# Kernel tuning notes

Measured on AMD Instinct MI355X. Metric: run time of the kernel, lower is better.

## Reference

```python
import jax, jax.numpy as jnp
import numpy as np

KERNEL_MUL = 2.0
KERNEL_NUM = 5


def setup_inputs() -> dict:
    key = jax.random.key(0)
    k1, k2 = jax.random.split(key)
    N, D = 4096, 512
    source = jax.random.normal(k1, (N, D), dtype=jnp.float32)
    target = jax.random.normal(k2, (N, D), dtype=jnp.float32)
    return {"source": source, "target": target}


def _mmd(source, target):
    n = source.shape[0]
    total = jnp.concatenate([source, target], axis=0)  # [2N, D]
    # pairwise squared L2 via the ||a||^2 + ||b||^2 - 2 a.b identity (same math,
    # avoids materializing the [2N,2N,D] expanded tensor the torch code builds)
    sq = jnp.sum(total * total, axis=1)  # [2N]
    L2 = sq[:, None] + sq[None, :] - 2.0 * (total @ total.T)  # [2N, 2N]
    m = total.shape[0]
    # torch uses L2_distance.data -> detached bandwidth
    bandwidth = jax.lax.stop_gradient(jnp.sum(L2)) / (m * m - m)
    bandwidth = bandwidth / (KERNEL_MUL ** (KERNEL_NUM // 2))
    kernels = jnp.zeros_like(L2)
    for i in range(KERNEL_NUM):
        kernels = kernels + jnp.exp(-L2 / (bandwidth * (KERNEL_MUL ** i)))
    XX = kernels[:n, :n]
    YY = kernels[n:, n:]
    XY = kernels[:n, n:]
    YX = kernels[n:, :n]
    return jnp.mean(XX + YY - XY - YX)


def reference(source, target):
    return _mmd(source, target)
```

## Files before the change

kernel.cpp:

```cpp
#include <hip/hip_runtime.h>
#include <hip/hip_fp8.h>

#define NHALF 4096
#define NROWS 8192
#define D 512
#define BM 128
#define BKB 128
#define NKT (D / BKB)
#define NB (NROWS / BM)
#define NTRI (NB * (NB + 1) / 2)
#define CONV_BLOCKS 256

typedef float f32x4 __attribute__((ext_vector_type(4)));

__device__ __forceinline__ const float* row_ptr(const float* __restrict__ src,
                                                const float* __restrict__ tgt, int r) {
    return (r < NHALF) ? (src + (size_t)r * D) : (tgt + (size_t)(r - NHALF) * D);
}

__global__ __launch_bounds__(256)
void conv_stats(const float* __restrict__ src, const float* __restrict__ tgt,
                unsigned char* __restrict__ tot8, float* __restrict__ sq,
                float* __restrict__ colsum, double* __restrict__ sumsq,
                unsigned* __restrict__ ticket, float* __restrict__ inv16bw_out) {
    __shared__ float cs_lds[4][512];
    __shared__ float wssq[4];
    __shared__ int lastFlag;
    __shared__ double red[256];
    int t = threadIdx.x, l = t & 63, w = t >> 6;
    int rbase = blockIdx.x * 32 + w * 8;

    float cs[8] = {0.f, 0.f, 0.f, 0.f, 0.f, 0.f, 0.f, 0.f};
    float ssq = 0.f;

    for (int rr = 0; rr < 8; ++rr) {
        int r = rbase + rr;
        const float* p = row_ptr(src, tgt, r) + l * 8;
        float4 v0 = *(const float4*)p;
        float4 v1 = *(const float4*)(p + 4);
        union { unsigned long long u; int i2[2]; } q;
        q.i2[0] = __builtin_amdgcn_cvt_pk_fp8_f32(v0.x, v0.y, 0, false);
        q.i2[0] = __builtin_amdgcn_cvt_pk_fp8_f32(v0.z, v0.w, q.i2[0], true);
        q.i2[1] = __builtin_amdgcn_cvt_pk_fp8_f32(v1.x, v1.y, 0, false);
        q.i2[1] = __builtin_amdgcn_cvt_pk_fp8_f32(v1.z, v1.w, q.i2[1], true);
        unsigned dstu = (unsigned)((l & 48) | ((l & 15) ^ (r & 15)));
        *(unsigned long long*)&tot8[(size_t)r * D + dstu * 8] = q.u;

        float s8 = v0.x*v0.x + v0.y*v0.y + v0.z*v0.z + v0.w*v0.w
                 + v1.x*v1.x + v1.y*v1.y + v1.z*v1.z + v1.w*v1.w;
        ssq += s8;
        cs[0] += v0.x; cs[1] += v0.y; cs[2] += v0.z; cs[3] += v0.w;
        cs[4] += v1.x; cs[5] += v1.y; cs[6] += v1.z; cs[7] += v1.w;
        float rsum = s8;
        for (int off = 32; off > 0; off >>= 1) rsum += __shfl_down(rsum, off);
        if (l == 0) sq[r] = rsum;
    }
#pragma unroll
    for (int j = 0; j < 8; ++j) cs_lds[w][l * 8 + j] = cs[j];
    for (int off = 32; off > 0; off >>= 1) ssq += __shfl_down(ssq, off);
    if (l == 0) wssq[w] = ssq;
    __syncthreads();
    int c0 = t * 2;
    float a = cs_lds[0][c0] + cs_lds[1][c0] + cs_lds[2][c0] + cs_lds[3][c0];
    float b = cs_lds[0][c0+1] + cs_lds[1][c0+1] + cs_lds[2][c0+1] + cs_lds[3][c0+1];
    atomicAdd(&colsum[c0], a);
    atomicAdd(&colsum[c0 + 1], b);
    if (t == 0) atomicAdd(sumsq, (double)(wssq[0] + wssq[1] + wssq[2] + wssq[3]));
    __syncthreads();

    if (t == 0) {
        __threadfence();
        unsigned old = atomicAdd(ticket, 1u);
        lastFlag = (old == CONV_BLOCKS - 1) ? 1 : 0;
    }
    __syncthreads();
    if (lastFlag) {
        float ca = atomicAdd(&colsum[t], 0.f);
        float cb = atomicAdd(&colsum[t + 256], 0.f);
        red[t] = (double)ca * ca + (double)cb * cb;
        __syncthreads();
        for (int s = 128; s > 0; s >>= 1) {
            if (t < s) red[t] += red[t + s];
            __syncthreads();
        }
        if (t == 0) {
            double ssqd = atomicAdd(sumsq, 0.0);
            double m = (double)NROWS;
            double sumL2 = 2.0 * m * ssqd - 2.0 * red[0];
            double bw = sumL2 / (m * m - m) / 4.0;
            inv16bw_out[0] = (float)(1.0 / (16.0 * bw));
        }
    }
}

__global__ __launch_bounds__(512, 4)
void mmd_main(const unsigned char* __restrict__ tot8,
              const float* __restrict__ sq, const float* __restrict__ inv16bw_p,
              double* __restrict__ S) {
    int b = blockIdx.x;
    int ti = (b & 7) * (NTRI / 8) + (b >> 3);
    int bi = (int)(64.5f - sqrtf(64.5f * 64.5f - 2.0f * (float)ti));
    if (bi < 0) bi = 0;
    while (bi > 0 && bi * NB - bi * (bi - 1) / 2 > ti) --bi;
    while ((bi + 1) * NB - (bi + 1) * bi / 2 <= ti) ++bi;
    int bj = bi + (ti - (bi * NB - bi * (bi - 1) / 2));

    __shared__ __align__(16) unsigned char As[BM * BKB];
    __shared__ __align__(16) unsigned char Bs[BM * BKB];

    int t = threadIdx.x, l = t & 63, w = t >> 6;
    int wr = w >> 2, wc = w & 3;
    int m = l & 15, kg = l >> 4;

    const unsigned char* ab = tot8 + (size_t)(bi * BM) * D;
    const unsigned char* bb = tot8 + (size_t)(bj * BM) * D;

    f32x4 acc[4][2];
#pragma unroll
    for (int i = 0; i < 4; ++i)
#pragma unroll
        for (int j = 0; j < 2; ++j)
            acc[i][j] = (f32x4){0.f, 0.f, 0.f, 0.f};

    for (int kt = 0; kt < NKT; ++kt) {
        __syncthreads();
#pragma unroll
        for (int i = 0; i < 2; ++i) {
            int g = i * 512 + t;
            int row = g >> 3, ch = g & 7;
            __builtin_amdgcn_global_load_lds(
                (const __attribute__((address_space(1))) void*)(ab + (size_t)row * D + kt * BKB + ch * 16),
                (__attribute__((address_space(3))) void*)(As + g * 16),
                16, 0, 0);
            __builtin_amdgcn_global_load_lds(
                (const __attribute__((address_space(1))) void*)(bb + (size_t)row * D + kt * BKB + ch * 16),
                (__attribute__((address_space(3))) void*)(Bs + g * 16),
                16, 0, 0);
        }
        __syncthreads();

#pragma unroll
        for (int ks = 0; ks < 4; ++ks) {
            long af[4], bfr[2];
#pragma unroll
            for (int fi = 0; fi < 4; ++fi) {
                int row = wr * 64 + fi * 16 + m;
                int unit = (ks * 4 + kg) ^ m;
                af[fi] = *(const long*)&As[row * BKB + unit * 8];
            }
#pragma unroll
            for (int fj = 0; fj < 2; ++fj) {
                int row = wc * 32 + fj * 16 + m;
                int unit = (ks * 4 + kg) ^ m;
                bfr[fj] = *(const long*)&Bs[row * BKB + unit * 8];
            }
#pragma unroll
            for (int fi = 0; fi < 4; ++fi)
#pragma unroll
                for (int fj = 0; fj < 2; ++fj)
                    acc[fi][fj] = __builtin_amdgcn_mfma_f32_16x16x32_fp8_fp8(af[fi], bfr[fj], acc[fi][fj], 0, 0, 0);
        }
    }

    float inv16bw = inv16bw_p[0];
    float coef = ((bi == bj) ? 1.f : 2.f) * (((bi < NB / 2) == (bj < NB / 2)) ? 1.f : -1.f);

    float sqj[2];
#pragma unroll
    for (int fj = 0; fj < 2; ++fj) sqj[fj] = sq[bj * BM + wc * 32 + fj * 16 + m];
    int ib = bi * BM + wr * 64 + kg * 4;

    float local = 0.f;
#pragma unroll
    for (int fi = 0; fi < 4; ++fi) {
        float sqi[4];
#pragma unroll
        for (int j = 0; j < 4; ++j) sqi[j] = sq[ib + fi * 16 + j];
#pragma unroll
        for (int fj = 0; fj < 2; ++fj) {
#pragma unroll
            for (int j = 0; j < 4; ++j) {
                float L2 = sqi[j] + sqj[fj] - 2.f * acc[fi][fj][j];
                float u = __expf(-L2 * inv16bw);
                float ks = u;
                u *= u; ks += u;
                u *= u; ks += u;
                u *= u; ks += u;
                u *= u; ks += u;
                if (bi == bj) {
                    int ig = wr * 64 + fi * 16 + kg * 4 + j;
                    int jg = wc * 32 + fj * 16 + m;
                    if (ig == jg) ks = 5.0f;
                }
                local += ks;
            }
        }
    }
    local *= coef;

    for (int off = 32; off > 0; off >>= 1) local += __shfl_down(local, off);
    __shared__ float wsum[8];
    if (l == 0) wsum[w] = local;
    __syncthreads();
    if (t == 0) {
        float bsum = wsum[0] + wsum[1] + wsum[2] + wsum[3]
                   + wsum[4] + wsum[5] + wsum[6] + wsum[7];
        atomicAdd(S, (double)bsum);
    }
}

__global__ void finalize_kernel(const double* __restrict__ S, float* __restrict__ out) {
    out[0] = (float)(S[0] / ((double)NHALF * (double)NHALF));
}

extern "C" void kernel_launch(void* const* d_in, const int* in_sizes, int n_in,
                              void* d_out, int out_size, void* d_ws, size_t ws_size,
                              hipStream_t stream) {
    const float* src = (const float*)d_in[0];
    const float* tgt = (const float*)d_in[1];
    float* out = (float*)d_out;
    char* ws = (char*)d_ws;

    unsigned char* tot8 = (unsigned char*)ws;
    float*    sq      = (float*)(ws + 4194304);
    float*    colsum  = (float*)(ws + 4194304 + 32768);
    double*   sumsq   = (double*)(ws + 4194304 + 34816);
    double*   S       = (double*)(ws + 4194304 + 34824);
    unsigned* ticket  = (unsigned*)(ws + 4194304 + 34832);
    float*    inv16bw = (float*)(ws + 4194304 + 34836);

    hipMemsetAsync(ws + 4194304 + 32768, 0, 2068, stream);

    conv_stats<<<CONV_BLOCKS, 256, 0, stream>>>(src, tgt, tot8, sq, colsum, sumsq, ticket, inv16bw);
    mmd_main<<<NTRI, 512, 0, stream>>>(tot8, sq, inv16bw, S);
    finalize_kernel<<<1, 1, 0, stream>>>(S, out);
}
```

Before: 74.18 us.

## Keep A row-panel resident in LDS and sweep four B tiles per block

Each block now loads its full 128x512 fp8 A row panel into LDS once and iterates over up to four column tiles of the upper triangle, streaming only B k-slices. The next tile's B staging is overlapped with the previous tile's exp epilogue, and per-block reductions become per-wave atomics. This cuts redundant A global loads and block count (2080 to 544). In exchange it uses 80KB of LDS per block, which lowers occupancy, and adds padding tiles clamped to bj=63 with zero coefficient, so some work is wasted.

```diff
diff --git a/kernel.cpp b/kernel.cpp
--- a/kernel.cpp
+++ b/kernel.cpp
@@ -8,7 +8,8 @@
 #define BKB 128
 #define NKT (D / BKB)
 #define NB (NROWS / BM)
-#define NTRI (NB * (NB + 1) / 2)
+#define TPB 4
+#define NBLK 544
 #define CONV_BLOCKS 256
 
 typedef float f32x4 __attribute__((ext_vector_type(4)));
@@ -98,115 +99,144 @@
               const float* __restrict__ sq, const float* __restrict__ inv16bw_p,
               double* __restrict__ S) {
     int b = blockIdx.x;
-    int ti = (b & 7) * (NTRI / 8) + (b >> 3);
-    int bi = (int)(64.5f - sqrtf(64.5f * 64.5f - 2.0f * (float)ti));
-    if (bi < 0) bi = 0;
-    while (bi > 0 && bi * NB - bi * (bi - 1) / 2 > ti) --bi;
-    while ((bi + 1) * NB - (bi + 1) * bi / 2 <= ti) ++bi;
-    int bj = bi + (ti - (bi * NB - bi * (bi - 1) / 2));
-
-    __shared__ __align__(16) unsigned char As[BM * BKB];
-    __shared__ __align__(16) unsigned char Bs[BM * BKB];
+    int nb = (b & 7) * (NBLK / 8) + (b >> 3);
+    int bi = 0, rem = nb;
+    while (rem >= ((67 - bi) >> 2)) { rem -= (67 - bi) >> 2; ++bi; }
+    int bj0 = bi + rem * 4;
+
+    __shared__ __align__(16) unsigned char Al[BM * D];
+    __shared__ __align__(16) unsigned char Bl[BM * BKB];
 
     int t = threadIdx.x, l = t & 63, w = t >> 6;
     int wr = w >> 2, wc = w & 3;
     int m = l & 15, kg = l >> 4;
 
-    const unsigned char* ab = tot8 + (size_t)(bi * BM) * D;
-    const unsigned char* bb = tot8 + (size_t)(bj * BM) * D;
-
-    f32x4 acc[4][2];
-#pragma unroll
-    for (int i = 0; i < 4; ++i)
-#pragma unroll
-        for (int j = 0; j < 2; ++j)
-            acc[i][j] = (f32x4){0.f, 0.f, 0.f, 0.f};
-
-    for (int kt = 0; kt < NKT; ++kt) {
-        __syncthreads();
+    const unsigned char* ap = tot8 + (size_t)bi * BM * D;
+
+    auto stage_B = [&](const unsigned char* bb, int kt) {
 #pragma unroll
         for (int i = 0; i < 2; ++i) {
             int g = i * 512 + t;
             int row = g >> 3, ch = g & 7;
             __builtin_amdgcn_global_load_lds(
-                (const __attribute__((address_space(1))) void*)(ab + (size_t)row * D + kt * BKB + ch * 16),
-                (__attribute__((address_space(3))) void*)(As + g * 16),
+                (const __attribute__((address_space(1))) void*)(bb + (size_t)row * D + kt * BKB + ch * 16),
+                (__attribute__((address_space(3))) void*)(Bl + g * 16),
                 16, 0, 0);
-            __builtin_amdgcn_global_load_lds(
-                (const __attribute__((address_space(1))) void*)(bb + (size_t)row * D + kt * BKB + ch * 16),
-                (__attribute__((address_space(3))) void*)(Bs + g * 16),
-                16, 0, 0);
-        }
-        __syncthreads();
-
-#pragma unroll
-        for (int ks = 0; ks < 4; ++ks) {
-            long af[4], bfr[2];
-#pragma unroll
-            for (int fi = 0; fi < 4; ++fi) {
-                int row = wr * 64 + fi * 16 + m;
+        }
+    };
+
+    f32x4 acc[4][2];
+#pragma unroll
+    for (int i = 0; i < 4; ++i)
+#pragma unroll
+        for (int j = 0; j < 2; ++j)
+            acc[i][j] = (f32x4){0.f, 0.f, 0.f, 0.f};
+
+#pragma unroll
+    for (int i = 0; i < 8; ++i) {
+        int g = i * 512 + t;
+        int row = g >> 5, ch = g & 31;
+        __builtin_amdgcn_global_load_lds(
+            (const __attribute__((address_space(1))) void*)(ap + (size_t)row * D + ch * 16),
+            (__attribute__((address_space(3))) void*)(Al + g * 16),
+            16, 0, 0);
+    }
+    const unsigned char* bb = tot8 + (size_t)bj0 * BM * D;
+    stage_B(bb, 0);
+    __syncthreads();
+
+    float inv16bw = inv16bw_p[0];
+    float wacc = 0.f;
+
+    auto epilogue = [&](int tile) {
+        int bjv = bj0 + tile;
+        float coef = 0.f;
+        int bjc = bjv;
+        if (bjv <= 63) {
+            coef = ((bi == bjv) ? 1.f : 2.f) * (((bi < 32) == (bjv < 32)) ? 1.f : -1.f);
+        } else bjc = 63;
+        float sqj[2];
+#pragma unroll
+        for (int fj = 0; fj < 2; ++fj) sqj[fj] = sq[bjc * BM + wc * 32 + fj * 16 + m];
+        int ib = bi * BM + wr * 64 + kg * 4;
+        float local = 0.f;
+#pragma unroll
+        for (int fi = 0; fi < 4; ++fi) {
+            float sqi[4];
+#pragma unroll
+            for (int j = 0; j < 4; ++j) sqi[j] = sq[ib + fi * 16 + j];
+#pragma unroll
+            for (int fj = 0; fj < 2; ++fj) {
+#pragma unroll
+                for (int j = 0; j < 4; ++j) {
+                    float L2 = sqi[j] + sqj[fj] - 2.f * acc[fi][fj][j];
+                    float u = __expf(-L2 * inv16bw);
+                    float ks = u;
+                    u *= u; ks += u;
+                    u *= u; ks += u;
+                    u *= u; ks += u;
+                    u *= u; ks += u;
+                    if (bi == bjc) {
+                        int ig = wr * 64 + fi * 16 + kg * 4 + j;
+                        int jg = wc * 32 + fj * 16 + m;
+                        if (ig == jg) ks = 5.0f;
+                    }
+                    local += ks;
+                }
+            }
+        }
+        local *= coef;
+        for (int off = 32; off > 0; off >>= 1) local += __shfl_down(local, off);
+        wacc += local;
+#pragma unroll
+        for (int i = 0; i < 4; ++i)
+#pragma unroll
+            for (int j = 0; j < 2; ++j)
+                acc[i][j] = (f32x4){0.f, 0.f, 0.f, 0.f};
+    };
+
+    for (int tp = 0; tp < TPB; ++tp) {
+        for (int kt = 0; kt < NKT; ++kt) {
+#pragma unroll
+            for (int ks = 0; ks < 4; ++ks) {
+                long af[4], bfr[2];
                 int unit = (ks * 4 + kg) ^ m;
-                af[fi] = *(const long*)&As[row * BKB + unit * 8];
+#pragma unroll
+                for (int fi = 0; fi < 4; ++fi) {
+                    int row = wr * 64 + fi * 16 + m;
+                    af[fi] = *(const long*)&Al[row * D + kt * BKB + unit * 8];
+                }
+#pragma unroll
+                for (int fj = 0; fj < 2; ++fj) {
+                    int row = wc * 32 + fj * 16 + m;
+                    bfr[fj] = *(const long*)&Bl[row * BKB + unit * 8];
+                }
+#pragma unroll
+                for (int fi = 0; fi < 4; ++fi)
+#pragma unroll
+                    for (int fj = 0; fj < 2; ++fj)
+                        acc[fi][fj] = __builtin_amdgcn_mfma_f32_16x16x32_fp8_fp8(af[fi], bfr[fj], acc[fi][fj], 0, 0, 0);
             }
-#pragma unroll
-            for (int fj = 0; fj < 2; ++fj) {
-                int row = wc * 32 + fj * 16 + m;
-                int unit = (ks * 4 + kg) ^ m;
-                bfr[fj] = *(const long*)&Bs[row * BKB + unit * 8];
+
+            bool lastStep = (tp == TPB - 1) && (kt == NKT - 1);
+            if (!lastStep) {
+                __syncthreads();
+                if (kt < NKT - 1) {
+                    stage_B(bb, kt + 1);
+                } else {
+                    int bjn = bj0 + tp + 1; if (bjn > 63) bjn = 63;
+                    bb = tot8 + (size_t)bjn * BM * D;
+                    stage_B(bb, 0);
+                    epilogue(tp);
+                }
+                __syncthreads();
+            } else {
+                epilogue(tp);
             }
-#pragma unroll
-            for (int fi = 0; fi < 4; ++fi)
-#pragma unroll
-                for (int fj = 0; fj < 2; ++fj)
-                    acc[fi][fj] = __builtin_amdgcn_mfma_f32_16x16x32_fp8_fp8(af[fi], bfr[fj], acc[fi][fj], 0, 0, 0);
-        }
-    }
-
-    float inv16bw = inv16bw_p[0];
-    float coef = ((bi == bj) ? 1.f : 2.f) * (((bi < NB / 2) == (bj < NB / 2)) ? 1.f : -1.f);
-
-    float sqj[2];
-#pragma unroll
-    for (int fj = 0; fj < 2; ++fj) sqj[fj] = sq[bj * BM + wc * 32 + fj * 16 + m];
-    int ib = bi * BM + wr * 64 + kg * 4;
-
-    float local = 0.f;
-#pragma unroll
-    for (int fi = 0; fi < 4; ++fi) {
-        float sqi[4];
-#pragma unroll
-        for (int j = 0; j < 4; ++j) sqi[j] = sq[ib + fi * 16 + j];
-#pragma unroll
-        for (int fj = 0; fj < 2; ++fj) {
-#pragma unroll
-            for (int j = 0; j < 4; ++j) {
-                float L2 = sqi[j] + sqj[fj] - 2.f * acc[fi][fj][j];
-                float u = __expf(-L2 * inv16bw);
-                float ks = u;
-                u *= u; ks += u;
-                u *= u; ks += u;
-                u *= u; ks += u;
-                u *= u; ks += u;
-                if (bi == bj) {
-                    int ig = wr * 64 + fi * 16 + kg * 4 + j;
-                    int jg = wc * 32 + fj * 16 + m;
-                    if (ig == jg) ks = 5.0f;
-                }
-                local += ks;
-            }
-        }
-    }
-    local *= coef;
-
-    for (int off = 32; off > 0; off >>= 1) local += __shfl_down(local, off);
-    __shared__ float wsum[8];
-    if (l == 0) wsum[w] = local;
-    __syncthreads();
-    if (t == 0) {
-        float bsum = wsum[0] + wsum[1] + wsum[2] + wsum[3]
-                   + wsum[4] + wsum[5] + wsum[6] + wsum[7];
-        atomicAdd(S, (double)bsum);
-    }
+        }
+    }
+
+    if (l == 0) atomicAdd(S, (double)wacc);
 }
 
 __global__ void finalize_kernel(const double* __restrict__ S, float* __restrict__ out) {
@@ -232,6 +262,6 @@
     hipMemsetAsync(ws + 4194304 + 32768, 0, 2068, stream);
 
     conv_stats<<<CONV_BLOCKS, 256, 0, stream>>>(src, tgt, tot8, sq, colsum, sumsq, ticket, inv16bw);
-    mmd_main<<<NTRI, 512, 0, stream>>>(tot8, sq, inv16bw, S);
+    mmd_main<<<NBLK, 512, 0, stream>>>(tot8, sq, inv16bw, S);
     finalize_kernel<<<1, 1, 0, stream>>>(S, out);
 }
```

Result: slower. 122.1 us (+64.6%).
